# Optimization experiments

Measured on AMD Instinct MI355X. Metric: run time of the kernel, lower is better.

Reference implementation:

```python
import jax, jax.numpy as jnp
import numpy as np

NEG_SLOPE = 0.2   # PyG GATConv default leaky_relu slope
K_TOP = 50        # img_token_len
EPS = 1e-12


def _add_self_loops(ei, n):
    loop = jnp.arange(n, dtype=ei.dtype)
    return jnp.concatenate([ei, jnp.stack([loop, loop])], axis=1)


def _gcn(x, ei, W, b, n):
    ei = _add_self_loops(ei, n)
    src, dst = ei[0], ei[1]
    deg = jax.ops.segment_sum(jnp.ones_like(src, jnp.float32), dst, num_segments=n)
    dinv = jax.lax.rsqrt(jnp.maximum(deg, EPS))
    norm = dinv[src] * dinv[dst]                      # [E+N]
    h = x @ W                                         # [N, H]
    out = jax.ops.segment_sum(h[src] * norm[:, None], dst, num_segments=n)
    return out + b


def _gat(x, ei, W, b, a_src, a_dst, n):
    # PyG GATConv, heads=1, concat=True, with self loops; returns attention
    ei = _add_self_loops(ei, n)
    src, dst = ei[0], ei[1]
    h = x @ W                                         # [N, D]
    asrc = h @ a_src                                  # [N]
    adst = h @ a_dst                                  # [N]
    e = jax.nn.leaky_relu(asrc[src] + adst[dst], NEG_SLOPE)
    # segment softmax over incoming edges of each dst node
    m = jax.ops.segment_max(e, dst, num_segments=n)
    ex = jnp.exp(e - m[dst])
    s = jax.ops.segment_sum(ex, dst, num_segments=n)
    alpha = ex / s[dst]                               # [E+N]
    out = jax.ops.segment_sum(alpha[:, None] * h[src], dst, num_segments=n) + b
    return out, ei, alpha


def _patch_att(ei, alpha, n):
    # fused form of the original per-edge python loop: scatter-add alpha to
    # both endpoints, count contributions, divide (segment mean)
    src, dst = ei[0], ei[1]
    ones = jnp.ones_like(alpha)
    att = jax.ops.segment_sum(alpha, src, num_segments=n) + \
          jax.ops.segment_sum(alpha, dst, num_segments=n)
    cnt = jax.ops.segment_sum(ones, src, num_segments=n) + \
          jax.ops.segment_sum(ones, dst, num_segments=n)
    return att / cnt


def reference(x, edge_index, W_gcn, b_gcn, W_gat, b_gat, a_src, a_dst, W_proj, b_proj):
    B, N, _ = x.shape

    def per_graph(xi, ei):
        h = jax.nn.relu(_gcn(xi, ei, W_gcn, b_gcn, N))        # dropout: eval mode (identity)
        gnn_out, ei_sl, alpha = _gat(h, ei, W_gat, b_gat, a_src, a_dst, N)
        score = _patch_att(ei_sl, alpha, N)
        return gnn_out, score

    emb, scores = jax.vmap(per_graph)(x, edge_index)          # [B,N,256], [B,N]
    emb = emb @ W_proj + b_proj                               # img_proj -> [B,N,1024]
    emb = emb.reshape(-1, emb.shape[-1])                      # [B*N, 1024]
    scores = scores.reshape(-1)                               # [B*N]
    topk_scores, topk_idx = jax.lax.top_k(scores, K_TOP)
    topk_feats = emb[topk_idx]                                # [50, 1024]
    return topk_feats


def setup_inputs() -> dict:
    key = jax.random.key(0)
    ks = jax.random.split(key, 8)
    B, N, E, F, H, D, P = 256, 100, 1600, 2048, 512, 256, 1024
    return {
        "x": jax.random.normal(ks[0], (B, N, F), jnp.float32),
        "edge_index": jax.random.randint(ks[1], (B, 2, E), 0, N, dtype=jnp.int64),
        "W_gcn": jax.random.normal(ks[2], (F, H), jnp.float32) * (1.0 / np.sqrt(F)),
        "b_gcn": jnp.zeros((H,), jnp.float32),
        "W_gat": jax.random.normal(ks[3], (H, D), jnp.float32) * (1.0 / np.sqrt(H)),
        "b_gat": jnp.zeros((D,), jnp.float32),
        "a_src": jax.random.normal(ks[4], (D,), jnp.float32) * 0.1,
        "a_dst": jax.random.normal(ks[5], (D,), jnp.float32) * 0.1,
        "W_proj": jax.random.normal(ks[6], (D, P), jnp.float32) * (1.0 / np.sqrt(D)),
        "b_proj": jnp.zeros((P,), jnp.float32),
    }
```

## Files before the change

### kernel.cpp

```cpp
#include <hip/hip_runtime.h>
#include <hip/hip_bf16.h>
#include <stdint.h>

#define NB      256
#define NN      100
#define NE      1600
#define NEL     1700
#define FIN     2048
#define HG      512
#define DG      256
#define PO      1024
#define KTOP    50
#define NEG_SLOPE 0.2f

typedef __attribute__((ext_vector_type(8))) short bf16x8;
typedef __attribute__((ext_vector_type(4))) float f32x4;

__device__ inline ushort f2bf(float x) {
  unsigned u = __float_as_uint(x);
  return (ushort)((u + 0x7fffu + ((u >> 16) & 1u)) >> 16);
}
__device__ inline float bf2f(ushort b) {
  return __uint_as_float((unsigned)b << 16);
}

template <int KSH>
__global__ void tsplit(const float* __restrict__ W, ushort* __restrict__ hiT,
                       ushort* __restrict__ loT, int N) {
  const int K = 1 << KSH;
  int e = blockIdx.x * 256 + threadIdx.x;
  if (e >= N * K) return;
  int n = e >> KSH, k = e & (K - 1);
  float v = W[(size_t)k * N + n];
  ushort h = f2bf(v);
  hiT[e] = h;
  loT[e] = f2bf(v - bf2f(h));
}

template <int BN, int KSH>
__global__ __launch_bounds__(256, 2) void gemm_split_mfma(
    const float* __restrict__ A, const ushort* __restrict__ Bhi_t,
    const ushort* __restrict__ Blo_t, float* __restrict__ C, int M, int N) {
  constexpr int K = 1 << KSH;
  constexpr int FN = BN / 32;
  __shared__ ushort Ahi[128 * 32], Alo[128 * 32];
  __shared__ ushort Bsh[BN * 32], Bsl[BN * 32];
  const int tid = threadIdx.x;
  const int lane = tid & 63;
  const int wid = tid >> 6;
  const int wm0 = (wid & 1) * 64;
  const int wn0 = (wid >> 1) * (BN / 2);
  const int bm0 = blockIdx.y * 128, bn0 = blockIdx.x * BN;
  const int r16 = lane & 15, g16 = lane >> 4;
  f32x4 acc[4][FN] = {};

  for (int k0 = 0; k0 < K; k0 += 32) {
    __syncthreads();
#pragma unroll
    for (int u = 0; u < 4; u++) {
      int c = tid + u * 256;
      int row = c >> 3, kc = (c & 7) * 4;
      float4 v = *(const float4*)&A[((size_t)(bm0 + row) << KSH) + k0 + kc];
      ushort4 h, l;
      h.x = f2bf(v.x); l.x = f2bf(v.x - bf2f(h.x));
      h.y = f2bf(v.y); l.y = f2bf(v.y - bf2f(h.y));
      h.z = f2bf(v.z); l.z = f2bf(v.z - bf2f(h.z));
      h.w = f2bf(v.w); l.w = f2bf(v.w - bf2f(h.w));
      *(ushort4*)&Ahi[row * 32 + kc] = h;
      *(ushort4*)&Alo[row * 32 + kc] = l;
    }
#pragma unroll
    for (int u = 0; u < BN / 64; u++) {
      int c = tid + u * 256;
      int col = c >> 2, kc = (c & 3) * 8;
      size_t gofs = ((size_t)(bn0 + col) << KSH) + k0 + kc;
      *(uint4*)&Bsh[col * 32 + kc] = *(const uint4*)&Bhi_t[gofs];
      *(uint4*)&Bsl[col * 32 + kc] = *(const uint4*)&Blo_t[gofs];
    }
    __syncthreads();
    bf16x8 ah[4], al[4];
#pragma unroll
    for (int m = 0; m < 4; m++) {
      ah[m] = *(const bf16x8*)&Ahi[(wm0 + m * 16 + r16) * 32 + g16 * 8];
      al[m] = *(const bf16x8*)&Alo[(wm0 + m * 16 + r16) * 32 + g16 * 8];
    }
#pragma unroll
    for (int n = 0; n < FN; n++) {
      bf16x8 bh = *(const bf16x8*)&Bsh[(wn0 + n * 16 + r16) * 32 + g16 * 8];
      bf16x8 bl = *(const bf16x8*)&Bsl[(wn0 + n * 16 + r16) * 32 + g16 * 8];
#pragma unroll
      for (int m = 0; m < 4; m++) {
        acc[m][n] = __builtin_amdgcn_mfma_f32_16x16x32_bf16(ah[m], bh, acc[m][n], 0, 0, 0);
        acc[m][n] = __builtin_amdgcn_mfma_f32_16x16x32_bf16(al[m], bh, acc[m][n], 0, 0, 0);
        acc[m][n] = __builtin_amdgcn_mfma_f32_16x16x32_bf16(ah[m], bl, acc[m][n], 0, 0, 0);
      }
    }
  }
  const int crow = g16 * 4;
#pragma unroll
  for (int m = 0; m < 4; m++)
#pragma unroll
    for (int n = 0; n < FN; n++)
#pragma unroll
      for (int r = 0; r < 4; r++)
        C[(size_t)(bm0 + wm0 + m * 16 + crow + r) * N + bn0 + wn0 + n * 16 + r16] =
            acc[m][n][r];
}

__global__ __launch_bounds__(512) void gcn_agg(
    const float* __restrict__ h0, const int* __restrict__ ei,
    const float* __restrict__ b_gcn, float* __restrict__ h1) {
  const int g = blockIdx.x, tid = threadIdx.x;
  __shared__ int   deg[NN];
  __shared__ float sdinv[NN];
  __shared__ int   offs[NN + 1], fill[NN];
  __shared__ int   eSrc[NEL];
  __shared__ float eNrm[NEL];
  const int* src = ei + (size_t)g * 2 * NE;
  const int* dst = src + NE;

  if (tid < NN) deg[tid] = 1;
  __syncthreads();
  for (int e = tid; e < NE; e += 512) atomicAdd(&deg[dst[e]], 1);
  __syncthreads();
  if (tid < NN) sdinv[tid] = rsqrtf(fmaxf((float)deg[tid], 1e-12f));
  if (tid == 0) {
    int s = 0;
    for (int n = 0; n < NN; n++) { offs[n] = s; s += deg[n]; }
    offs[NN] = s;
  }
  __syncthreads();
  if (tid < NN) fill[tid] = offs[tid];
  __syncthreads();
  for (int e = tid; e < NE; e += 512) {
    int s = src[e], d = dst[e];
    int p = atomicAdd(&fill[d], 1);
    eSrc[p] = s;
    eNrm[p] = sdinv[s] * sdinv[d];
  }
  if (tid < NN) {
    int p = atomicAdd(&fill[tid], 1);
    eSrc[p] = tid;
    eNrm[p] = sdinv[tid] * sdinv[tid];
  }
  __syncthreads();

  const float* h0g = h0 + (size_t)g * NN * HG;
  float* h1g = h1 + (size_t)g * NN * HG;
  const int grp = tid >> 7, tf = tid & 127;
  float4 bias = *(const float4*)&b_gcn[tf * 4];
  for (int n = grp; n < NN; n += 4) {
    float4 acc = bias;
    const int p1 = offs[n + 1];
    for (int p = offs[n]; p < p1; p++) {
      float nr = eNrm[p];
      float4 hv = *(const float4*)&h0g[(size_t)eSrc[p] * HG + tf * 4];
      acc.x = fmaf(hv.x, nr, acc.x);
      acc.y = fmaf(hv.y, nr, acc.y);
      acc.z = fmaf(hv.z, nr, acc.z);
      acc.w = fmaf(hv.w, nr, acc.w);
    }
    acc.x = fmaxf(acc.x, 0.f); acc.y = fmaxf(acc.y, 0.f);
    acc.z = fmaxf(acc.z, 0.f); acc.w = fmaxf(acc.w, 0.f);
    *(float4*)&h1g[(size_t)n * HG + tf * 4] = acc;
  }
}

__device__ inline unsigned fmap(float f) {
  unsigned b = __float_as_uint(f);
  return (b & 0x80000000u) ? ~b : (b | 0x80000000u);
}
__device__ inline float funmap(unsigned u) {
  return __uint_as_float((u & 0x80000000u) ? (u & 0x7fffffffu) : ~u);
}

__global__ __launch_bounds__(256) void gat_kernel(
    const float* __restrict__ h2, const int* __restrict__ ei,
    const float* __restrict__ a_src, const float* __restrict__ a_dst,
    const float* __restrict__ b_gat, float* __restrict__ out,
    float* __restrict__ scores) {
  const int g = blockIdx.x, tid = threadIdx.x;
  __shared__ float    sAs[NN], sAd[NN];
  __shared__ unsigned mKey[NN];
  __shared__ float    sSum[NN], sAtt[NN];
  __shared__ int      sCnt[NN], degl[NN];
  __shared__ int      offs[NN + 1], fill[NN];
  __shared__ float    eV[NEL];
  __shared__ int      eS[NEL];
  __shared__ float    eA[NEL];
  const int* src = ei + (size_t)g * 2 * NE;
  const int* dst = src + NE;
  const float* h2g = h2 + (size_t)g * NN * DG;

  const int lane = tid & 63, wv = tid >> 6;
  for (int n = wv; n < NN; n += 4) {
    float4 hv  = *(const float4*)&h2g[(size_t)n * DG + lane * 4];
    float4 as4 = *(const float4*)&a_src[lane * 4];
    float4 ad4 = *(const float4*)&a_dst[lane * 4];
    float ps = hv.x * as4.x + hv.y * as4.y + hv.z * as4.z + hv.w * as4.w;
    float pd = hv.x * ad4.x + hv.y * ad4.y + hv.z * ad4.z + hv.w * ad4.w;
#pragma unroll
    for (int o = 32; o; o >>= 1) {
      ps += __shfl_down(ps, o);
      pd += __shfl_down(pd, o);
    }
    if (lane == 0) { sAs[n] = ps; sAd[n] = pd; }
  }
  if (tid < NN) {
    mKey[tid] = 0u; sSum[tid] = 0.f; sAtt[tid] = 0.f;
    sCnt[tid] = 0;  degl[tid] = 1;
  }
  __syncthreads();

  for (int i = tid; i < NEL; i += 256) {
    int s, d;
    if (i < NE) { s = src[i]; d = dst[i]; } else { s = d = i - NE; }
    float e = sAs[s] + sAd[d];
    e = (e > 0.f) ? e : NEG_SLOPE * e;
    eV[i] = e;
    atomicMax(&mKey[d], fmap(e));
    if (i < NE) atomicAdd(&degl[d], 1);
  }
  __syncthreads();

  for (int i = tid; i < NEL; i += 256) {
    int d = (i < NE) ? dst[i] : i - NE;
    float ex = expf(eV[i] - funmap(mKey[d]));
    eV[i] = ex;
    atomicAdd(&sSum[d], ex);
  }
  if (tid == 0) {
    int s = 0;
    for (int n = 0; n < NN; n++) { offs[n] = s; s += degl[n]; }
    offs[NN] = s;
  }
  __syncthreads();
  if (tid < NN) fill[tid] = offs[tid];
  __syncthreads();

  for (int i = tid; i < NEL; i += 256) {
    int s, d;
    if (i < NE) { s = src[i]; d = dst[i]; } else { s = d = i - NE; }
    float al = eV[i] / sSum[d];
    atomicAdd(&sAtt[s], al);
    atomicAdd(&sAtt[d], al);
    atomicAdd(&sCnt[s], 1);
    atomicAdd(&sCnt[d], 1);
    int p = atomicAdd(&fill[d], 1);
    eS[p] = s;
    eA[p] = al;
  }
  __syncthreads();

  if (tid < NN) scores[g * NN + tid] = sAtt[tid] / (float)sCnt[tid];

  float* outg = out + (size_t)g * NN * DG;
  const int grp = tid >> 6, tf = tid & 63;
  float4 bias = *(const float4*)&b_gat[tf * 4];
  for (int n = grp; n < NN; n += 4) {
    float4 acc = bias;
    const int p1 = offs[n + 1];
    for (int p = offs[n]; p < p1; p++) {
      float al = eA[p];
      float4 hv = *(const float4*)&h2g[(size_t)eS[p] * DG + tf * 4];
      acc.x = fmaf(hv.x, al, acc.x);
      acc.y = fmaf(hv.y, al, acc.y);
      acc.z = fmaf(hv.z, al, acc.z);
      acc.w = fmaf(hv.w, al, acc.w);
    }
    *(float4*)&outg[(size_t)n * DG + tf * 4] = acc;
  }
}

__global__ __launch_bounds__(1024) void topk_radix(
    const float* __restrict__ scores, int* __restrict__ topk) {
  const int tid = threadIdx.x;
  unsigned key[25];
#pragma unroll
  for (int u = 0; u < 25; u++) key[u] = fmap(scores[tid + u * 1024]);

  __shared__ unsigned hist[16][256];
  __shared__ unsigned total[256];
  __shared__ unsigned sPref;
  __shared__ int sNeed;
  const int wv = tid >> 6;
  unsigned pref = 0;
  int plen = 0, need = KTOP;
  for (int pass = 0; pass < 4; pass++) {
    const int shift = 24 - 8 * pass;
    for (int i = tid; i < 16 * 256; i += 1024) ((unsigned*)hist)[i] = 0;
    __syncthreads();
#pragma unroll
    for (int u = 0; u < 25; u++) {
      unsigned k = key[u];
      bool ok = (plen == 0) || ((k >> (32 - plen)) == (pref >> (32 - plen)));
      if (ok) atomicAdd(&hist[wv][(k >> shift) & 255], 1u);
    }
    __syncthreads();
    if (tid < 256) {
      unsigned s = 0;
      for (int w = 0; w < 16; w++) s += hist[w][tid];
      total[tid] = s;
    }
    __syncthreads();
    if (tid == 0) {
      unsigned cum = 0;
      int b = 255;
      for (; b > 0; b--) {
        cum += total[b];
        if ((int)cum >= need) break;
      }
      if ((int)cum < need) cum += total[0];
      sPref = pref | ((unsigned)b << shift);
      sNeed = need - (int)(cum - total[b]);
    }
    __syncthreads();
    pref = sPref;
    need = sNeed;
    plen += 8;
    __syncthreads();
  }

  const unsigned thr = pref;
  __shared__ int nGt;
  __shared__ unsigned long long cand[64];
  __shared__ int eqMin;
  if (tid == 0) nGt = 0;
  __syncthreads();
  unsigned eqmask = 0;
#pragma unroll
  for (int u = 0; u < 25; u++) {
    unsigned k = key[u];
    if (k > thr) {
      int p = atomicAdd(&nGt, 1);
      cand[p] = ((unsigned long long)k << 32) | (unsigned)(~(tid + u * 1024));
    } else if (k == thr) {
      eqmask |= 1u << u;
    }
  }
  __syncthreads();
  const int base = nGt;
  for (int r = 0; r < need; r++) {
    if (tid == 0) eqMin = 0x7fffffff;
    __syncthreads();
    int mymin = 0x7fffffff;
    unsigned mm = eqmask;
    while (mm) {
      int u = __ffs(mm) - 1;
      mm &= mm - 1;
      int idx = tid + u * 1024;
      if (idx < mymin) mymin = idx;
    }
#pragma unroll
    for (int o = 32; o; o >>= 1) {
      int ot = __shfl_down(mymin, o);
      if (ot < mymin) mymin = ot;
    }
    if ((tid & 63) == 0 && mymin != 0x7fffffff) atomicMin(&eqMin, mymin);
    __syncthreads();
    int sel = eqMin;
    if (tid == 0) topk[base + r] = sel;
    if ((sel & 1023) == tid) eqmask &= ~(1u << (sel >> 10));
    __syncthreads();
  }
  if (tid < 64) {
    unsigned long long c = (tid < base) ? cand[tid] : 0ull;
    for (int r = 0; r < base; r++) {
      unsigned long long m = c;
#pragma unroll
      for (int o = 32; o; o >>= 1) {
        unsigned long long t2 = __shfl_down(m, o);
        if (t2 > m) m = t2;
      }
      m = __shfl(m, 0);
      if (tid == 0) topk[r] = (int)(~(unsigned)m);
      if (c == m) c = 0ull;
    }
  }
}

__global__ __launch_bounds__(256) void proj_kernel(
    const float* __restrict__ gnn, const int* __restrict__ topk,
    const float* __restrict__ Wp, const float* __restrict__ bp,
    float* __restrict__ outp) {
  const int bi = blockIdx.x >> 2;
  const int c0 = (blockIdx.x & 3) * 256;
  const int tid = threadIdx.x;
  __shared__ float row[DG];
  const int node = topk[bi];
  row[tid] = gnn[(size_t)node * DG + tid];
  __syncthreads();
  float acc = 0.f;
  for (int k = 0; k < DG; k++)
    acc = fmaf(row[k], Wp[(size_t)k * PO + c0 + tid], acc);
  outp[(size_t)bi * PO + c0 + tid] = acc + bp[c0 + tid];
}

extern "C" void kernel_launch(void* const* d_in, const int* in_sizes, int n_in,
                              void* d_out, int out_size, void* d_ws,
                              size_t ws_size, hipStream_t stream) {
  const float* x      = (const float*)d_in[0];
  const int*   ei     = (const int*)d_in[1];
  const float* W_gcn  = (const float*)d_in[2];
  const float* b_gcn  = (const float*)d_in[3];
  const float* W_gat  = (const float*)d_in[4];
  const float* b_gat  = (const float*)d_in[5];
  const float* a_src  = (const float*)d_in[6];
  const float* a_dst  = (const float*)d_in[7];
  const float* W_proj = (const float*)d_in[8];
  const float* b_proj = (const float*)d_in[9];
  float* outp = (float*)d_out;

  char* ws = (char*)d_ws;
  float*  h0       = (float*)ws;
  float*  h2       = (float*)ws;
  float*  gnn      = (float*)(ws + 26214400);
  float*  h1       = (float*)(ws + 52428800);
  char*   wsc      = ws + 104857600;
  ushort* WgcnT_hi = (ushort*)(wsc);
  ushort* WgcnT_lo = (ushort*)(wsc + 2097152);
  ushort* WgatT_hi = (ushort*)(wsc + 4194304);
  ushort* WgatT_lo = (ushort*)(wsc + 4456448);
  float*  scores   = (float*)(wsc + 4718592);
  int*    topk     = (int*)(wsc + 4820992);

  const int M = NB * NN;

  tsplit<11><<<(HG * FIN + 255) / 256, 256, 0, stream>>>(W_gcn, WgcnT_hi,
                                                         WgcnT_lo, HG);
  tsplit<9><<<(DG * HG + 255) / 256, 256, 0, stream>>>(W_gat, WgatT_hi,
                                                       WgatT_lo, DG);
  gemm_split_mfma<256, 11><<<dim3(HG / 256, M / 128), 256, 0, stream>>>(
      x, WgcnT_hi, WgcnT_lo, h0, M, HG);
  gcn_agg<<<NB, 512, 0, stream>>>(h0, ei, b_gcn, h1);
  gemm_split_mfma<128, 9><<<dim3(DG / 128, M / 128), 256, 0, stream>>>(
      h1, WgatT_hi, WgatT_lo, h2, M, DG);
  gat_kernel<<<NB, 256, 0, stream>>>(h2, ei, a_src, a_dst, b_gat, gnn, scores);
  topk_radix<<<1, 1024, 0, stream>>>(scores, topk);
  proj_kernel<<<KTOP * 4, 256, 0, stream>>>(gnn, topk, W_proj, b_proj, outp);
}
```

Before: 774.8 us.

## Use async LDS loads with swizzle in GEMM and split aggregation kernels across feature chunks

The split-bf16 GEMM now uses a fixed 128x128 tile with 3 blocks per CU as the occupancy target. B tiles are loaded straight into LDS with global_load_lds, and an XOR swizzle is applied to the LDS layout to avoid bank conflicts. GCN aggregation is split across 4 feature-chunk blocks per graph. GAT is split into an alpha/CSR kernel and a separate aggregation kernel over 2 feature chunks, which raises parallelism beyond 256 blocks. The cost is redundant CSR construction per chunk, an extra global round trip for CSR data, and more register pressure.

```diff
diff --git a/kernel.cpp b/kernel.cpp
--- a/kernel.cpp
+++ b/kernel.cpp
@@ -15,6 +15,7 @@
 
 typedef __attribute__((ext_vector_type(8))) short bf16x8;
 typedef __attribute__((ext_vector_type(4))) float f32x4;
+typedef unsigned int u32;
 
 __device__ inline ushort f2bf(float x) {
   unsigned u = __float_as_uint(x);
@@ -22,6 +23,16 @@
 }
 __device__ inline float bf2f(ushort b) {
   return __uint_as_float((unsigned)b << 16);
+}
+
+__device__ inline void gl16(const void* g, void* l) {
+  __builtin_amdgcn_global_load_lds(
+      (const __attribute__((address_space(1))) u32*)g,
+      (__attribute__((address_space(3))) u32*)l, 16, 0, 0);
+}
+
+__device__ inline int swz(int row, int kc) {
+  return row * 32 + ((((kc >> 3) ^ (row & 3)) << 3) | (kc & 7));
 }
 
 template <int KSH>
@@ -37,57 +48,68 @@
   loT[e] = f2bf(v - bf2f(h));
 }
 
-template <int BN, int KSH>
-__global__ __launch_bounds__(256, 2) void gemm_split_mfma(
+template <int KSH>
+__global__ __launch_bounds__(256, 3) void gemm_split_mfma(
     const float* __restrict__ A, const ushort* __restrict__ Bhi_t,
     const ushort* __restrict__ Blo_t, float* __restrict__ C, int M, int N) {
   constexpr int K = 1 << KSH;
-  constexpr int FN = BN / 32;
   __shared__ ushort Ahi[128 * 32], Alo[128 * 32];
-  __shared__ ushort Bsh[BN * 32], Bsl[BN * 32];
+  __shared__ ushort Bsh[128 * 32], Bsl[128 * 32];
   const int tid = threadIdx.x;
   const int lane = tid & 63;
   const int wid = tid >> 6;
   const int wm0 = (wid & 1) * 64;
-  const int wn0 = (wid >> 1) * (BN / 2);
-  const int bm0 = blockIdx.y * 128, bn0 = blockIdx.x * BN;
+  const int wn0 = (wid >> 1) * 64;
+  const int bm0 = blockIdx.y * 128, bn0 = blockIdx.x * 128;
   const int r16 = lane & 15, g16 = lane >> 4;
-  f32x4 acc[4][FN] = {};
+  f32x4 acc[4][4] = {};
+
+  const int bcol0 = wid * 32 + (lane >> 2);
+  const int g_log0 = (lane & 3) ^ (bcol0 & 3);
+  const int bcol1 = bcol0 + 16;
+  const int g_log1 = (lane & 3) ^ (bcol1 & 3);
 
   for (int k0 = 0; k0 < K; k0 += 32) {
     __syncthreads();
+    {
+      size_t go0 = (((size_t)(bn0 + bcol0)) << KSH) + k0 + g_log0 * 8;
+      size_t go1 = (((size_t)(bn0 + bcol1)) << KSH) + k0 + g_log1 * 8;
+      ushort* lb0 = &Bsh[(wid * 32) * 32];
+      ushort* lb1 = &Bsh[(wid * 32 + 16) * 32];
+      ushort* lc0 = &Bsl[(wid * 32) * 32];
+      ushort* lc1 = &Bsl[(wid * 32 + 16) * 32];
+      gl16(&Bhi_t[go0], lb0);
+      gl16(&Bhi_t[go1], lb1);
+      gl16(&Blo_t[go0], lc0);
+      gl16(&Blo_t[go1], lc1);
+    }
 #pragma unroll
     for (int u = 0; u < 4; u++) {
       int c = tid + u * 256;
       int row = c >> 3, kc = (c & 7) * 4;
-      float4 v = *(const float4*)&A[((size_t)(bm0 + row) << KSH) + k0 + kc];
+      float4 v = *(const float4*)&A[(((size_t)(bm0 + row)) << KSH) + k0 + kc];
       ushort4 h, l;
       h.x = f2bf(v.x); l.x = f2bf(v.x - bf2f(h.x));
       h.y = f2bf(v.y); l.y = f2bf(v.y - bf2f(h.y));
       h.z = f2bf(v.z); l.z = f2bf(v.z - bf2f(h.z));
       h.w = f2bf(v.w); l.w = f2bf(v.w - bf2f(h.w));
-      *(ushort4*)&Ahi[row * 32 + kc] = h;
-      *(ushort4*)&Alo[row * 32 + kc] = l;
-    }
-#pragma unroll
-    for (int u = 0; u < BN / 64; u++) {
-      int c = tid + u * 256;
-      int col = c >> 2, kc = (c & 3) * 8;
-      size_t gofs = ((size_t)(bn0 + col) << KSH) + k0 + kc;
-      *(uint4*)&Bsh[col * 32 + kc] = *(const uint4*)&Bhi_t[gofs];
-      *(uint4*)&Bsl[col * 32 + kc] = *(const uint4*)&Blo_t[gofs];
+      int o = swz(row, kc);
+      *(ushort4*)&Ahi[o] = h;
+      *(ushort4*)&Alo[o] = l;
     }
     __syncthreads();
     bf16x8 ah[4], al[4];
 #pragma unroll
     for (int m = 0; m < 4; m++) {
-      ah[m] = *(const bf16x8*)&Ahi[(wm0 + m * 16 + r16) * 32 + g16 * 8];
-      al[m] = *(const bf16x8*)&Alo[(wm0 + m * 16 + r16) * 32 + g16 * 8];
-    }
-#pragma unroll
-    for (int n = 0; n < FN; n++) {
-      bf16x8 bh = *(const bf16x8*)&Bsh[(wn0 + n * 16 + r16) * 32 + g16 * 8];
-      bf16x8 bl = *(const bf16x8*)&Bsl[(wn0 + n * 16 + r16) * 32 + g16 * 8];
+      int o = swz(wm0 + m * 16 + r16, g16 * 8);
+      ah[m] = *(const bf16x8*)&Ahi[o];
+      al[m] = *(const bf16x8*)&Alo[o];
+    }
+#pragma unroll
+    for (int n = 0; n < 4; n++) {
+      int o = swz(wn0 + n * 16 + r16, g16 * 8);
+      bf16x8 bh = *(const bf16x8*)&Bsh[o];
+      bf16x8 bl = *(const bf16x8*)&Bsl[o];
 #pragma unroll
       for (int m = 0; m < 4; m++) {
         acc[m][n] = __builtin_amdgcn_mfma_f32_16x16x32_bf16(ah[m], bh, acc[m][n], 0, 0, 0);
@@ -100,17 +122,17 @@
 #pragma unroll
   for (int m = 0; m < 4; m++)
 #pragma unroll
-    for (int n = 0; n < FN; n++)
+    for (int n = 0; n < 4; n++)
 #pragma unroll
       for (int r = 0; r < 4; r++)
         C[(size_t)(bm0 + wm0 + m * 16 + crow + r) * N + bn0 + wn0 + n * 16 + r16] =
             acc[m][n][r];
 }
 
-__global__ __launch_bounds__(512) void gcn_agg(
+__global__ __launch_bounds__(256) void gcn_agg(
     const float* __restrict__ h0, const int* __restrict__ ei,
     const float* __restrict__ b_gcn, float* __restrict__ h1) {
-  const int g = blockIdx.x, tid = threadIdx.x;
+  const int g = blockIdx.x, fc0 = blockIdx.y * 128, tid = threadIdx.x;
   __shared__ int   deg[NN];
   __shared__ float sdinv[NN];
   __shared__ int   offs[NN + 1], fill[NN];
@@ -121,7 +143,7 @@
 
   if (tid < NN) deg[tid] = 1;
   __syncthreads();
-  for (int e = tid; e < NE; e += 512) atomicAdd(&deg[dst[e]], 1);
+  for (int e = tid; e < NE; e += 256) atomicAdd(&deg[dst[e]], 1);
   __syncthreads();
   if (tid < NN) sdinv[tid] = rsqrtf(fmaxf((float)deg[tid], 1e-12f));
   if (tid == 0) {
@@ -132,7 +154,7 @@
   __syncthreads();
   if (tid < NN) fill[tid] = offs[tid];
   __syncthreads();
-  for (int e = tid; e < NE; e += 512) {
+  for (int e = tid; e < NE; e += 256) {
     int s = src[e], d = dst[e];
     int p = atomicAdd(&fill[d], 1);
     eSrc[p] = s;
@@ -145,11 +167,11 @@
   }
   __syncthreads();
 
-  const float* h0g = h0 + (size_t)g * NN * HG;
-  float* h1g = h1 + (size_t)g * NN * HG;
-  const int grp = tid >> 7, tf = tid & 127;
-  float4 bias = *(const float4*)&b_gcn[tf * 4];
-  for (int n = grp; n < NN; n += 4) {
+  const float* h0g = h0 + (size_t)g * NN * HG + fc0;
+  float* h1g = h1 + (size_t)g * NN * HG + fc0;
+  const int grp = tid >> 5, tf = tid & 31;
+  float4 bias = *(const float4*)&b_gcn[fc0 + tf * 4];
+  for (int n = grp; n < NN; n += 8) {
     float4 acc = bias;
     const int p1 = offs[n + 1];
     for (int p = offs[n]; p < p1; p++) {
@@ -174,11 +196,11 @@
   return __uint_as_float((u & 0x80000000u) ? (u & 0x7fffffffu) : ~u);
 }
 
-__global__ __launch_bounds__(256) void gat_kernel(
+__global__ __launch_bounds__(256) void gat_alpha(
     const float* __restrict__ h2, const int* __restrict__ ei,
     const float* __restrict__ a_src, const float* __restrict__ a_dst,
-    const float* __restrict__ b_gat, float* __restrict__ out,
-    float* __restrict__ scores) {
+    float* __restrict__ scores, int* __restrict__ csrO,
+    int* __restrict__ csrS, float* __restrict__ csrA) {
   const int g = blockIdx.x, tid = threadIdx.x;
   __shared__ float    sAs[NN], sAd[NN];
   __shared__ unsigned mKey[NN];
@@ -253,11 +275,33 @@
   __syncthreads();
 
   if (tid < NN) scores[g * NN + tid] = sAtt[tid] / (float)sCnt[tid];
-
-  float* outg = out + (size_t)g * NN * DG;
-  const int grp = tid >> 6, tf = tid & 63;
-  float4 bias = *(const float4*)&b_gat[tf * 4];
-  for (int n = grp; n < NN; n += 4) {
+  if (tid <= NN) csrO[g * (NN + 1) + tid] = offs[tid];
+  for (int i = tid; i < NEL; i += 256) {
+    csrS[(size_t)g * NEL + i] = eS[i];
+    csrA[(size_t)g * NEL + i] = eA[i];
+  }
+}
+
+__global__ __launch_bounds__(256) void gat_agg(
+    const float* __restrict__ h2, const int* __restrict__ csrO,
+    const int* __restrict__ csrS, const float* __restrict__ csrA,
+    const float* __restrict__ b_gat, float* __restrict__ out) {
+  const int g = blockIdx.x, fc0 = blockIdx.y * 128, tid = threadIdx.x;
+  __shared__ int   offs[NN + 1];
+  __shared__ int   eS[NEL];
+  __shared__ float eA[NEL];
+  if (tid <= NN) offs[tid] = csrO[g * (NN + 1) + tid];
+  for (int i = tid; i < NEL; i += 256) {
+    eS[i] = csrS[(size_t)g * NEL + i];
+    eA[i] = csrA[(size_t)g * NEL + i];
+  }
+  __syncthreads();
+
+  const float* h2g = h2 + (size_t)g * NN * DG + fc0;
+  float* outg = out + (size_t)g * NN * DG + fc0;
+  const int grp = tid >> 5, tf = tid & 31;
+  float4 bias = *(const float4*)&b_gat[fc0 + tf * 4];
+  for (int n = grp; n < NN; n += 8) {
     float4 acc = bias;
     const int p1 = offs[n + 1];
     for (int p = offs[n]; p < p1; p++) {
@@ -423,6 +467,9 @@
   ushort* WgatT_lo = (ushort*)(wsc + 4456448);
   float*  scores   = (float*)(wsc + 4718592);
   int*    topk     = (int*)(wsc + 4820992);
+  int*    csrO     = (int*)(wsc + 4823040);
+  int*    csrS     = (int*)(wsc + 4926464);
+  float*  csrA     = (float*)(wsc + 6667264);
 
   const int M = NB * NN;
 
@@ -430,12 +477,14 @@
                                                          WgcnT_lo, HG);
   tsplit<9><<<(DG * HG + 255) / 256, 256, 0, stream>>>(W_gat, WgatT_hi,
                                                        WgatT_lo, DG);
-  gemm_split_mfma<256, 11><<<dim3(HG / 256, M / 128), 256, 0, stream>>>(
+  gemm_split_mfma<11><<<dim3(HG / 128, M / 128), 256, 0, stream>>>(
       x, WgcnT_hi, WgcnT_lo, h0, M, HG);
-  gcn_agg<<<NB, 512, 0, stream>>>(h0, ei, b_gcn, h1);
-  gemm_split_mfma<128, 9><<<dim3(DG / 128, M / 128), 256, 0, stream>>>(
+  gcn_agg<<<dim3(NB, 4), 256, 0, stream>>>(h0, ei, b_gcn, h1);
+  gemm_split_mfma<9><<<dim3(DG / 128, M / 128), 256, 0, stream>>>(
       h1, WgatT_hi, WgatT_lo, h2, M, DG);
-  gat_kernel<<<NB, 256, 0, stream>>>(h2, ei, a_src, a_dst, b_gat, gnn, scores);
+  gat_alpha<<<NB, 256, 0, stream>>>(h2, ei, a_src, a_dst, scores, csrO, csrS,
+                                    csrA);
+  gat_agg<<<dim3(NB, 2), 256, 0, stream>>>(h2, csrO, csrS, csrA, b_gat, gnn);
   topk_radix<<<1, 1024, 0, stream>>>(scores, topk);
   proj_kernel<<<KTOP * 4, 256, 0, stream>>>(gnn, topk, W_proj, b_proj, outp);
 }
```

After: 820.4 us. 5.9% more time.
